# Performance work log

Hardware: AMD Instinct MI355X
Metric: run time of the kernel (lower is better)

The kernel has to match this reference:

```python
import jax, jax.numpy as jnp
import numpy as np

N_NODES = 100000
HIDDEN = 512
NUM_GRAPHS = 1024


def setup_inputs() -> dict:
    key = jax.random.key(0)
    k_h, k_b, k_w1, k_w2 = jax.random.split(key, 4)
    s1 = 1.0 / np.sqrt(HIDDEN)
    return {
        "h": jax.random.normal(k_h, (N_NODES, HIDDEN), dtype=jnp.float32),
        "batch_vec": jnp.sort(jax.random.randint(k_b, (N_NODES,), 0, NUM_GRAPHS, dtype=jnp.int32)),
        "W1": jax.random.normal(k_w1, (HIDDEN, HIDDEN), dtype=jnp.float32) * s1,
        "b1": jnp.zeros((HIDDEN,), dtype=jnp.float32),
        "W2": jax.random.normal(k_w2, (HIDDEN, 1), dtype=jnp.float32) * s1,
        "b2": jnp.zeros((1,), dtype=jnp.float32),
    }


def reference(h, batch_vec, W1, b1, W2, b2):
    # gate MLP (Dropout is identity in eval): [N, hidden] -> [N]
    gate = (jax.nn.gelu(h @ W1 + b1, approximate=False) @ W2 + b2)[:, 0]
    # segment softmax over graphs (batch_vec)
    m = jax.ops.segment_max(gate, batch_vec, num_segments=NUM_GRAPHS)
    e = jnp.exp(gate - m[batch_vec])
    denom = jax.ops.segment_sum(e, batch_vec, num_segments=NUM_GRAPHS)
    alpha = e / denom[batch_vec]  # [N]
    # scatter-weighted sum: [num_graphs, hidden]
    return jax.ops.segment_sum(alpha[:, None] * h, batch_vec, num_segments=NUM_GRAPHS)
```

## Files before the change

kernel.cpp:

```cpp
#include <hip/hip_runtime.h>
#include <hip/hip_bf16.h>
#include <float.h>

#define N_NODES 100000
#define HID     512
#define NGRAPH  1024
#define BM      48
#define NRB     ((N_NODES + BM - 1) / BM)
#define GRID    256

typedef __bf16 bf16_t;
typedef bf16_t bf16x8 __attribute__((ext_vector_type(8)));
typedef float  f32x4  __attribute__((ext_vector_type(4)));

__device__ __forceinline__ float fast_gelu(float x) {
    const float z = __builtin_fabsf(x) * 0.70710678118654752f;
    const float t = __fdividef(1.0f, __builtin_fmaf(0.3275911f, z, 1.0f));
    float p = __builtin_fmaf(1.061405429f, t, -1.453152027f);
    p = __builtin_fmaf(p, t, 1.421413741f);
    p = __builtin_fmaf(p, t, -0.284496736f);
    p = __builtin_fmaf(p, t, 0.254829592f);
    p *= t;
    const float e    = __expf(-z * z);
    const float erfz = __builtin_fmaf(-p, e, 1.0f);
    const float s    = __builtin_copysignf(erfz, x);
    return 0.5f * x * (1.0f + s);
}

__global__ void __launch_bounds__(256) k_w1t_tiled(const float* __restrict__ w1,
                                                   bf16_t* __restrict__ bt) {
    const int u   = blockIdx.x * 256 + threadIdx.x;
    const int col = u & 511;
    const int g4  = u >> 9;
    const int k0  = g4 * 8;
    bf16x8 v;
    #pragma unroll
    for (int e = 0; e < 8; ++e)
        v[e] = (bf16_t)w1[(size_t)(k0 + e) * HID + col];
    *reinterpret_cast<bf16x8*>(bt + (size_t)u * 8) = v;
}

__global__ void __launch_bounds__(1024, 4) k_gemm_gate(const float* __restrict__ h,
                                                       const bf16_t* __restrict__ bt,
                                                       const float* __restrict__ b1,
                                                       const float* __restrict__ w2,
                                                       const float* __restrict__ b2,
                                                       float* __restrict__ gate) {
    __shared__ __align__(16) bf16_t As[2][BM * HID];
    __shared__ float gp[16][BM];

    const int tid  = threadIdx.x;
    const int lane = tid & 63;
    const int wv   = tid >> 6;
    const int l15  = lane & 15;
    const int l4   = lane >> 4;

    float b1v[2], w2v[2];
    #pragma unroll
    for (int nf = 0; nf < 2; ++nf) {
        const int cg = wv * 32 + nf * 16 + l15;
        b1v[nf] = b1[cg];
        w2v[nf] = w2[cg];
    }
    const float b2v = b2[0];

    const bf16_t* bbase = bt + ((size_t)l4 * 512 + wv * 32 + l15) * 8;

    {
        const int rb = blockIdx.x;
        #pragma unroll
        for (int i = 0; i < 3; ++i) {
            const int idx = i * 1024 + tid;
            const int row = idx >> 6;
            const int cu  = idx & 63;
            const int grow = rb * BM + row;
            f32x4 s0 = f32x4{0.f, 0.f, 0.f, 0.f}, s1 = s0;
            if (grow < N_NODES) {
                const f32x4* p = reinterpret_cast<const f32x4*>(
                    h + (size_t)grow * HID + cu * 8);
                s0 = p[0]; s1 = p[1];
            }
            bf16x8 v;
            #pragma unroll
            for (int j = 0; j < 4; ++j) { v[j] = (bf16_t)s0[j]; v[4 + j] = (bf16_t)s1[j]; }
            *reinterpret_cast<bf16x8*>(
                (char*)&As[0][0] + row * 1024 + ((cu ^ (row & 7)) * 16)) = v;
        }
    }
    __syncthreads();

    int cur = 0;
    for (int rb = blockIdx.x; rb < NRB; rb += GRID) {
        const int  rbn  = rb + GRID;
        const bool have = rbn < NRB;

        f32x4 st[6];
        if (have) {
            #pragma unroll
            for (int i = 0; i < 3; ++i) {
                const int idx = i * 1024 + tid;
                const int row = idx >> 6;
                const int cu  = idx & 63;
                const int grow = rbn * BM + row;
                f32x4 s0 = f32x4{0.f, 0.f, 0.f, 0.f}, s1 = s0;
                if (grow < N_NODES) {
                    const f32x4* p = reinterpret_cast<const f32x4*>(
                        h + (size_t)grow * HID + cu * 8);
                    s0 = p[0]; s1 = p[1];
                }
                st[2 * i] = s0; st[2 * i + 1] = s1;
            }
        }

        const char* abase = (const char*)&As[cur][0] + l15 * 1024;
        f32x4 acc[3][2] = {};
        bf16x8 breg[2][2];
        #pragma unroll
        for (int nf = 0; nf < 2; ++nf)
            breg[0][nf] = *reinterpret_cast<const bf16x8*>(bbase + nf * 128);
        #pragma unroll
        for (int nf = 0; nf < 2; ++nf)
            breg[1][nf] = *reinterpret_cast<const bf16x8*>(bbase + 16384 + nf * 128);
        #pragma unroll 4
        for (int kt = 0; kt < 16; ++kt) {
            const int chunkoff = ((kt * 4 + l4) ^ (l15 & 7)) * 16;
            bf16x8 af[3];
            #pragma unroll
            for (int mf = 0; mf < 3; ++mf)
                af[mf] = *reinterpret_cast<const bf16x8*>(
                    abase + mf * 16384 + chunkoff);
            #pragma unroll
            for (int mf = 0; mf < 3; ++mf)
                #pragma unroll
                for (int nf = 0; nf < 2; ++nf)
                    acc[mf][nf] = __builtin_amdgcn_mfma_f32_16x16x32_bf16(
                        af[mf], breg[kt & 1][nf], acc[mf][nf], 0, 0, 0);
            if (kt < 14) {
                #pragma unroll
                for (int nf = 0; nf < 2; ++nf)
                    breg[kt & 1][nf] = *reinterpret_cast<const bf16x8*>(
                        bbase + (size_t)(kt + 2) * 16384 + nf * 128);
            }
        }

        if (have) {
            #pragma unroll
            for (int i = 0; i < 3; ++i) {
                const int idx = i * 1024 + tid;
                const int row = idx >> 6;
                const int cu  = idx & 63;
                bf16x8 v;
                #pragma unroll
                for (int j = 0; j < 4; ++j) { v[j] = (bf16_t)st[2*i][j]; v[4+j] = (bf16_t)st[2*i+1][j]; }
                *reinterpret_cast<bf16x8*>(
                    (char*)&As[cur ^ 1][0] + row * 1024 + ((cu ^ (row & 7)) * 16)) = v;
            }
        }

        float pr[12];
        #pragma unroll
        for (int i = 0; i < 12; ++i) pr[i] = 0.f;
        #pragma unroll
        for (int nf = 0; nf < 2; ++nf) {
            #pragma unroll
            for (int mf = 0; mf < 3; ++mf) {
                #pragma unroll
                for (int rr = 0; rr < 4; ++rr) {
                    const float ge = fast_gelu(acc[mf][nf][rr] + b1v[nf]);
                    pr[mf * 4 + rr] = fmaf(ge, w2v[nf], pr[mf * 4 + rr]);
                }
            }
        }
        #pragma unroll
        for (int i = 0; i < 12; ++i) {
            float v = pr[i];
            v += __shfl_xor(v, 1);
            v += __shfl_xor(v, 2);
            v += __shfl_xor(v, 4);
            v += __shfl_xor(v, 8);
            pr[i] = v;
        }
        __syncthreads();
        if (l15 == 0) {
            #pragma unroll
            for (int mf = 0; mf < 3; ++mf)
                #pragma unroll
                for (int rr = 0; rr < 4; ++rr)
                    gp[wv][mf * 16 + l4 * 4 + rr] = pr[mf * 4 + rr];
        }
        __syncthreads();
        if (tid < BM) {
            const int grow = rb * BM + tid;
            if (grow < N_NODES) {
                float s = b2v;
                #pragma unroll
                for (int w = 0; w < 16; ++w) s += gp[w][tid];
                gate[grow] = s;
            }
        }
        cur ^= 1;
    }
}

__global__ void __launch_bounds__(256) k_pool(const float* __restrict__ h,
                                              const int* __restrict__ bv,
                                              const float* __restrict__ gate,
                                              float* __restrict__ out) {
    const int g   = blockIdx.x;
    const int tid = threadIdx.x;
    __shared__ int   s_bounds[2];
    __shared__ float s_red[4];
    __shared__ float s_alpha[256];

    if (tid == 0) {
        int lo = 0, hi = N_NODES;
        while (lo < hi) { int mid = (lo + hi) >> 1; if (bv[mid] < g) lo = mid + 1; else hi = mid; }
        s_bounds[0] = lo;
        int lo2 = lo, hi2 = N_NODES;
        while (lo2 < hi2) { int mid = (lo2 + hi2) >> 1; if (bv[mid] < g + 1) lo2 = mid + 1; else hi2 = mid; }
        s_bounds[1] = lo2;
    }
    __syncthreads();
    const int start = s_bounds[0], end = s_bounds[1];

    float2 acc = make_float2(0.f, 0.f);
    if (start < end) {
        const int lane = tid & 63, wv = tid >> 6;
        float lm = -FLT_MAX;
        for (int i = start + tid; i < end; i += 256) lm = fmaxf(lm, gate[i]);
        #pragma unroll
        for (int o = 32; o; o >>= 1) lm = fmaxf(lm, __shfl_xor(lm, o));
        if (lane == 0) s_red[wv] = lm;
        __syncthreads();
        const float m = fmaxf(fmaxf(s_red[0], s_red[1]), fmaxf(s_red[2], s_red[3]));
        __syncthreads();
        float ls = 0.f;
        for (int i = start + tid; i < end; i += 256) ls += expf(gate[i] - m);
        #pragma unroll
        for (int o = 32; o; o >>= 1) ls += __shfl_xor(ls, o);
        if (lane == 0) s_red[wv] = ls;
        __syncthreads();
        const float inv = 1.f / (s_red[0] + s_red[1] + s_red[2] + s_red[3]);
        const float* hcol = h + tid * 2;
        for (int base = start; base < end; base += 256) {
            const int j = base + tid;
            const float av = (j < end) ? expf(gate[j] - m) * inv : 0.f;
            __syncthreads();
            s_alpha[tid] = av;
            __syncthreads();
            const int cnt = min(256, end - base);
            for (int jj = 0; jj < cnt; ++jj) {
                const float a = s_alpha[jj];
                const float2 hv = *reinterpret_cast<const float2*>(
                    hcol + (size_t)(base + jj) * HID);
                acc.x = fmaf(a, hv.x, acc.x);
                acc.y = fmaf(a, hv.y, acc.y);
            }
        }
    }
    *reinterpret_cast<float2*>(out + (size_t)g * HID + tid * 2) = acc;
}

extern "C" void kernel_launch(void* const* d_in, const int* in_sizes, int n_in,
                              void* d_out, int out_size, void* d_ws, size_t ws_size,
                              hipStream_t stream) {
    const float* h  = (const float*)d_in[0];
    const int*   bv = (const int*)d_in[1];
    const float* W1 = (const float*)d_in[2];
    const float* b1 = (const float*)d_in[3];
    const float* W2 = (const float*)d_in[4];
    const float* b2 = (const float*)d_in[5];
    float* out = (float*)d_out;

    char* ws = (char*)d_ws;
    bf16_t* bt   = (bf16_t*)ws;
    float*  gate = (float*)(ws + 524288);

    k_w1t_tiled<<<dim3(128), dim3(256), 0, stream>>>(W1, bt);
    k_gemm_gate<<<dim3(GRID), dim3(1024), 0, stream>>>(h, bt, b1, W2, b2, gate);
    k_pool<<<dim3(NGRAPH), dim3(256), 0, stream>>>(h, bv, gate, out);
}
```

Baseline: 151.6 us.

## Split GEMM N dimension across block pairs and keep W1 slice register-resident

The gate GEMM now gives each pair of blocks one 48-row tile, with each block covering half of the 512 hidden columns using 512 threads. Each block loads its whole W1 slice into registers once instead of streaming it from global/L2 on every tile. The A tile goes from double-buffered to single-buffered LDS, with the next-tile store moved after the compute. Partial gate sums are written per half and combined in a new small reduce kernel. The costs are that every h tile is read and converted twice, there is an extra launch, and register pressure from the 32 resident B vectors is high.

```diff
diff --git a/kernel.cpp b/kernel.cpp
--- a/kernel.cpp
+++ b/kernel.cpp
@@ -7,7 +7,7 @@
 #define NGRAPH  1024
 #define BM      48
 #define NRB     ((N_NODES + BM - 1) / BM)
-#define GRID    256
+#define GRID    512
 
 typedef __bf16 bf16_t;
 typedef bf16_t bf16x8 __attribute__((ext_vector_type(8)));
@@ -40,14 +40,13 @@
     *reinterpret_cast<bf16x8*>(bt + (size_t)u * 8) = v;
 }
 
-__global__ void __launch_bounds__(1024, 4) k_gemm_gate(const float* __restrict__ h,
-                                                       const bf16_t* __restrict__ bt,
-                                                       const float* __restrict__ b1,
-                                                       const float* __restrict__ w2,
-                                                       const float* __restrict__ b2,
-                                                       float* __restrict__ gate) {
-    __shared__ __align__(16) bf16_t As[2][BM * HID];
-    __shared__ float gp[16][BM];
+__global__ void __launch_bounds__(512, 2) k_gemm_gate(const float* __restrict__ h,
+                                                      const bf16_t* __restrict__ bt,
+                                                      const float* __restrict__ b1,
+                                                      const float* __restrict__ w2,
+                                                      float* __restrict__ gpart) {
+    __shared__ __align__(16) bf16_t As[BM * HID];
+    __shared__ float gp[8][BM];
 
     const int tid  = threadIdx.x;
     const int lane = tid & 63;
@@ -55,50 +54,57 @@
     const int l15  = lane & 15;
     const int l4   = lane >> 4;
 
+    const int nh    = blockIdx.x & 1;
+    const int start = blockIdx.x >> 1;
+
+    const bf16_t* bbase = bt + ((size_t)l4 * 512 + nh * 256 + wv * 32 + l15) * 8;
+    bf16x8 breg[16][2];
+    #pragma unroll
+    for (int kt = 0; kt < 16; ++kt)
+        #pragma unroll
+        for (int nf = 0; nf < 2; ++nf)
+            breg[kt][nf] = *reinterpret_cast<const bf16x8*>(
+                bbase + (size_t)kt * 16384 + nf * 128);
+
     float b1v[2], w2v[2];
     #pragma unroll
     for (int nf = 0; nf < 2; ++nf) {
-        const int cg = wv * 32 + nf * 16 + l15;
+        const int cg = nh * 256 + wv * 32 + nf * 16 + l15;
         b1v[nf] = b1[cg];
         w2v[nf] = w2[cg];
     }
-    const float b2v = b2[0];
-
-    const bf16_t* bbase = bt + ((size_t)l4 * 512 + wv * 32 + l15) * 8;
-
-    {
-        const int rb = blockIdx.x;
-        #pragma unroll
-        for (int i = 0; i < 3; ++i) {
-            const int idx = i * 1024 + tid;
-            const int row = idx >> 6;
-            const int cu  = idx & 63;
-            const int grow = rb * BM + row;
-            f32x4 s0 = f32x4{0.f, 0.f, 0.f, 0.f}, s1 = s0;
-            if (grow < N_NODES) {
-                const f32x4* p = reinterpret_cast<const f32x4*>(
-                    h + (size_t)grow * HID + cu * 8);
-                s0 = p[0]; s1 = p[1];
-            }
-            bf16x8 v;
-            #pragma unroll
-            for (int j = 0; j < 4; ++j) { v[j] = (bf16_t)s0[j]; v[4 + j] = (bf16_t)s1[j]; }
-            *reinterpret_cast<bf16x8*>(
-                (char*)&As[0][0] + row * 1024 + ((cu ^ (row & 7)) * 16)) = v;
-        }
+
+    #pragma unroll
+    for (int i = 0; i < 6; ++i) {
+        const int idx = i * 512 + tid;
+        const int row = idx >> 6;
+        const int cu  = idx & 63;
+        const int grow = start * BM + row;
+        f32x4 s0 = f32x4{0.f, 0.f, 0.f, 0.f}, s1 = s0;
+        if (grow < N_NODES) {
+            const f32x4* p = reinterpret_cast<const f32x4*>(
+                h + (size_t)grow * HID + cu * 8);
+            s0 = p[0]; s1 = p[1];
+        }
+        bf16x8 v;
+        #pragma unroll
+        for (int j = 0; j < 4; ++j) { v[j] = (bf16_t)s0[j]; v[4 + j] = (bf16_t)s1[j]; }
+        *reinterpret_cast<bf16x8*>(
+            (char*)As + row * 1024 + ((cu ^ (row & 7)) * 16)) = v;
     }
     __syncthreads();
 
-    int cur = 0;
-    for (int rb = blockIdx.x; rb < NRB; rb += GRID) {
-        const int  rbn  = rb + GRID;
+    const char* abase = (const char*)As + l15 * 1024;
+
+    for (int rb = start; rb < NRB; rb += 256) {
+        const int  rbn  = rb + 256;
         const bool have = rbn < NRB;
 
-        f32x4 st[6];
+        f32x4 st[12];
         if (have) {
             #pragma unroll
-            for (int i = 0; i < 3; ++i) {
-                const int idx = i * 1024 + tid;
+            for (int i = 0; i < 6; ++i) {
+                const int idx = i * 512 + tid;
                 const int row = idx >> 6;
                 const int cu  = idx & 63;
                 const int grow = rbn * BM + row;
@@ -112,16 +118,8 @@
             }
         }
 
-        const char* abase = (const char*)&As[cur][0] + l15 * 1024;
         f32x4 acc[3][2] = {};
-        bf16x8 breg[2][2];
-        #pragma unroll
-        for (int nf = 0; nf < 2; ++nf)
-            breg[0][nf] = *reinterpret_cast<const bf16x8*>(bbase + nf * 128);
-        #pragma unroll
-        for (int nf = 0; nf < 2; ++nf)
-            breg[1][nf] = *reinterpret_cast<const bf16x8*>(bbase + 16384 + nf * 128);
-        #pragma unroll 4
+        #pragma unroll
         for (int kt = 0; kt < 16; ++kt) {
             const int chunkoff = ((kt * 4 + l4) ^ (l15 & 7)) * 16;
             bf16x8 af[3];
@@ -134,27 +132,7 @@
                 #pragma unroll
                 for (int nf = 0; nf < 2; ++nf)
                     acc[mf][nf] = __builtin_amdgcn_mfma_f32_16x16x32_bf16(
-                        af[mf], breg[kt & 1][nf], acc[mf][nf], 0, 0, 0);
-            if (kt < 14) {
-                #pragma unroll
-                for (int nf = 0; nf < 2; ++nf)
-                    breg[kt & 1][nf] = *reinterpret_cast<const bf16x8*>(
-                        bbase + (size_t)(kt + 2) * 16384 + nf * 128);
-            }
-        }
-
-        if (have) {
-            #pragma unroll
-            for (int i = 0; i < 3; ++i) {
-                const int idx = i * 1024 + tid;
-                const int row = idx >> 6;
-                const int cu  = idx & 63;
-                bf16x8 v;
-                #pragma unroll
-                for (int j = 0; j < 4; ++j) { v[j] = (bf16_t)st[2*i][j]; v[4+j] = (bf16_t)st[2*i+1][j]; }
-                *reinterpret_cast<bf16x8*>(
-                    (char*)&As[cur ^ 1][0] + row * 1024 + ((cu ^ (row & 7)) * 16)) = v;
-            }
+                        af[mf], breg[kt][nf], acc[mf][nf], 0, 0, 0);
         }
 
         float pr[12];
@@ -180,6 +158,7 @@
             v += __shfl_xor(v, 8);
             pr[i] = v;
         }
+
         __syncthreads();
         if (l15 == 0) {
             #pragma unroll
@@ -187,19 +166,38 @@
                 #pragma unroll
                 for (int rr = 0; rr < 4; ++rr)
                     gp[wv][mf * 16 + l4 * 4 + rr] = pr[mf * 4 + rr];
+        }
+        if (have) {
+            #pragma unroll
+            for (int i = 0; i < 6; ++i) {
+                const int idx = i * 512 + tid;
+                const int row = idx >> 6;
+                const int cu  = idx & 63;
+                bf16x8 v;
+                #pragma unroll
+                for (int j = 0; j < 4; ++j) { v[j] = (bf16_t)st[2*i][j]; v[4+j] = (bf16_t)st[2*i+1][j]; }
+                *reinterpret_cast<bf16x8*>(
+                    (char*)As + row * 1024 + ((cu ^ (row & 7)) * 16)) = v;
+            }
         }
         __syncthreads();
         if (tid < BM) {
             const int grow = rb * BM + tid;
             if (grow < N_NODES) {
-                float s = b2v;
-                #pragma unroll
-                for (int w = 0; w < 16; ++w) s += gp[w][tid];
-                gate[grow] = s;
-            }
-        }
-        cur ^= 1;
-    }
+                float s = 0.f;
+                #pragma unroll
+                for (int w = 0; w < 8; ++w) s += gp[w][tid];
+                gpart[(size_t)nh * N_NODES + grow] = s;
+            }
+        }
+    }
+}
+
+__global__ void __launch_bounds__(256) k_gate_reduce(const float* __restrict__ gpart,
+                                                     const float* __restrict__ b2,
+                                                     float* __restrict__ gate) {
+    int i = blockIdx.x * 256 + threadIdx.x;
+    if (i < N_NODES) gate[i] = gpart[i] + gpart[N_NODES + i] + b2[0];
 }
 
 __global__ void __launch_bounds__(256) k_pool(const float* __restrict__ h,
@@ -273,10 +271,12 @@
     float* out = (float*)d_out;
 
     char* ws = (char*)d_ws;
-    bf16_t* bt   = (bf16_t*)ws;
-    float*  gate = (float*)(ws + 524288);
+    bf16_t* bt    = (bf16_t*)ws;
+    float*  gpart = (float*)(ws + 524288);
+    float*  gate  = (float*)(ws + 524288 + 800000);
 
     k_w1t_tiled<<<dim3(128), dim3(256), 0, stream>>>(W1, bt);
-    k_gemm_gate<<<dim3(GRID), dim3(1024), 0, stream>>>(h, bt, b1, W2, b2, gate);
+    k_gemm_gate<<<dim3(GRID), dim3(512), 0, stream>>>(h, bt, b1, W2, gpart);
+    k_gate_reduce<<<dim3((N_NODES + 255) / 256), dim3(256), 0, stream>>>(gpart, b2, gate);
     k_pool<<<dim3(NGRAPH), dim3(256), 0, stream>>>(h, bv, gate, out);
 }
```

Result: slower. 186.4 us (+22.9%).
